# Performance work log

Hardware: AMD Instinct MI355X
Metric: run time of the kernel (lower is better)

The kernel has to match this reference:

```python
import jax, jax.numpy as jnp
import numpy as np

T, B, OBS, H, FC = 128, 512, 1024, 512, 512
LN_EPS = 1e-6  # flax LayerNorm default


def setup_inputs() -> dict:
    key = jax.random.key(0)
    ks = jax.random.split(key, 8)
    sc = lambda k, shape, s: jax.random.normal(k, shape, jnp.float32) * s
    return dict(
        hidden=jnp.zeros((B, H), jnp.float32),  # GRUCell.initialize_carry -> zeros
        world_state=jax.random.normal(ks[0], (T, B, OBS), jnp.float32),
        dones=jax.random.bernoulli(ks[1], 0.05, (T, B)),
        Wd=sc(ks[2], (OBS, H), 1.0 / np.sqrt(OBS)),
        bd=jnp.zeros((H,), jnp.float32),
        ln_scale=jnp.ones((H,), jnp.float32),
        ln_bias=jnp.zeros((H,), jnp.float32),
        Wi=sc(ks[3], (H, 3 * H), 1.0 / np.sqrt(H)),  # input-side GRU weights [r|z|n]
        bi=jnp.zeros((3 * H,), jnp.float32),
        Wh=sc(ks[4], (H, 3 * H), 1.0 / np.sqrt(H)),  # hidden-side GRU weights [r|z|n]
        bhn=jnp.zeros((H,), jnp.float32),            # flax GRU: only hn dense has bias
        Wc1=sc(ks[5], (H, FC), 1.0 / np.sqrt(H)),
        bc1=jnp.zeros((FC,), jnp.float32),
        Wc2=sc(ks[6], (FC, 1), 1.0 / np.sqrt(FC)),
        bc2=jnp.zeros((1,), jnp.float32),
    )


def reference(hidden, world_state, dones, Wd, bd, ln_scale, ln_bias,
              Wi, bi, Wh, bhn, Wc1, bc1, Wc2, bc2):
    # Embed: Dense -> relu -> LayerNorm, applied to all timesteps at once
    emb = jax.nn.relu(world_state @ Wd + bd)                      # [T,B,H]
    mu = emb.mean(-1, keepdims=True)
    var = ((emb - mu) ** 2).mean(-1, keepdims=True)
    emb = (emb - mu) * jax.lax.rsqrt(var + LN_EPS) * ln_scale + ln_bias

    # Precompute input-side GRU projections for all steps (hoisted out of scan)
    xproj = emb @ Wi + bi                                         # [T,B,3H]

    def step(h, inputs):
        xp, done = inputs
        h = jnp.where(done[:, None], 0.0, h)                      # reset carry on done
        xr, xz, xn = jnp.split(xp, 3, axis=-1)
        hr, hz, hn = jnp.split(h @ Wh, 3, axis=-1)                # [B,H] each
        r = jax.nn.sigmoid(xr + hr)
        z = jax.nn.sigmoid(xz + hz)
        n = jnp.tanh(xn + r * (hn + bhn))
        h_new = (1.0 - z) * n + z * h
        return h_new, h_new

    h_last, ys = jax.lax.scan(step, hidden, (xproj, dones))       # ys: [T,B,H]

    critic = jax.nn.relu(ys @ Wc1 + bc1)                          # [T,B,FC]
    value = jnp.squeeze(critic @ Wc2 + bc2, axis=-1)              # [T,B]
    return h_last, value
```

## Files before the change

kernel.cpp:

```cpp
#include <hip/hip_runtime.h>
#include <stdint.h>

#define T_STEPS 128
#define BATCH   512
#define OBSD    1024
#define HD      512
#define FCD     512
#define MROWS   (T_STEPS * BATCH)

typedef unsigned short ushort_t;
typedef __attribute__((ext_vector_type(8))) short bf16x8;
typedef __attribute__((ext_vector_type(4))) float f32x4;

__device__ inline ushort_t f2bf(float f) {
    union { float f; uint32_t u; } v; v.f = f;
    uint32_t r = v.u + 0x7FFFu + ((v.u >> 16) & 1u);
    return (ushort_t)(r >> 16);
}
__device__ inline float bf2f(ushort_t h) {
    union { uint32_t u; float f; } v; v.u = ((uint32_t)h) << 16;
    return v.f;
}
__device__ inline float fsigmoid(float x) {
    x = fminf(fmaxf(x, -30.f), 30.f);
    return 1.f / (1.f + __expf(-x));
}
__device__ inline float ftanh(float x) {
    float e = __expf(fminf(fmaxf(2.f * x, -30.f), 30.f));
    return (e - 1.f) / (e + 1.f);
}

__global__ void transpose_to_bf16(const float* __restrict__ in,
                                  ushort_t* __restrict__ out, int R, int C) {
    __shared__ float tile[32][33];
    int tx = threadIdx.x, ty = threadIdx.y;
    int c0 = blockIdx.x * 32, r0 = blockIdx.y * 32;
    for (int yy = 0; yy < 4; ++yy)
        tile[ty + 8 * yy][tx] = in[(size_t)(r0 + ty + 8 * yy) * C + c0 + tx];
    __syncthreads();
    for (int yy = 0; yy < 4; ++yy)
        out[(size_t)(c0 + ty + 8 * yy) * R + r0 + tx] = f2bf(tile[tx][ty + 8 * yy]);
}

__global__ void init_misc(float* __restrict__ v, const float* __restrict__ bc2,
                          unsigned* __restrict__ bar) {
    int i = blockIdx.x * blockDim.x + threadIdx.x;
    if (i < MROWS) v[i] = bc2[0];
    if (i < 2048) bar[i] = 0u;
}

template <int K, int EPI, bool AF32>
__global__ __launch_bounds__(256) void gemm64(
    const void* __restrict__ Aptr, const ushort_t* __restrict__ BT,
    const float* __restrict__ bias, ushort_t* __restrict__ Cout, int ldc,
    const float* __restrict__ wc2, float* __restrict__ value) {
    __shared__ __align__(16) ushort_t Als[64][40];
    __shared__ __align__(16) ushort_t Bls[64][40];
    int tid = threadIdx.x;
    int wave = tid >> 6, lane = tid & 63, quad = lane >> 4, l16 = lane & 15;
    int bm = blockIdx.x * 64, bn = blockIdx.y * 64;
    int lrow = tid >> 2, lk = (tid & 3) * 8;

    f32x4 acc[4];
    for (int c = 0; c < 4; ++c) acc[c] = (f32x4){0.f, 0.f, 0.f, 0.f};

    for (int k0 = 0; k0 < K; k0 += 32) {
        if constexpr (AF32) {
            const float* A = (const float*)Aptr;
            const float4* pa =
                (const float4*)&A[(size_t)(bm + lrow) * K + k0 + lk];
            float4 a0 = pa[0], a1 = pa[1];
            ushort_t* d = &Als[lrow][lk];
            d[0] = f2bf(a0.x); d[1] = f2bf(a0.y); d[2] = f2bf(a0.z); d[3] = f2bf(a0.w);
            d[4] = f2bf(a1.x); d[5] = f2bf(a1.y); d[6] = f2bf(a1.z); d[7] = f2bf(a1.w);
        } else {
            const ushort_t* A = (const ushort_t*)Aptr;
            *(bf16x8*)&Als[lrow][lk] =
                *(const bf16x8*)&A[(size_t)(bm + lrow) * K + k0 + lk];
        }
        *(bf16x8*)&Bls[lrow][lk] =
            *(const bf16x8*)&BT[(size_t)(bn + lrow) * K + k0 + lk];
        __syncthreads();
        bf16x8 a = *(const bf16x8*)&Als[16 * wave + l16][quad * 8];
        for (int c = 0; c < 4; ++c) {
            bf16x8 b = *(const bf16x8*)&Bls[16 * c + l16][quad * 8];
            acc[c] = __builtin_amdgcn_mfma_f32_16x16x32_bf16(a, b, acc[c], 0, 0, 0);
        }
        __syncthreads();
    }

    int row_l = 16 * wave + 4 * quad;
    if constexpr (EPI == 0 || EPI == 1) {
        for (int c = 0; c < 4; ++c) {
            int col = bn + 16 * c + l16;
            float bv = bias[col];
            for (int i = 0; i < 4; ++i) {
                float v = acc[c][i] + bv;
                if constexpr (EPI == 0) v = fmaxf(v, 0.f);
                Cout[(size_t)(bm + row_l + i) * ldc + col] = f2bf(v);
            }
        }
    } else {
        float s[4] = {0.f, 0.f, 0.f, 0.f};
        for (int c = 0; c < 4; ++c) {
            int col = bn + 16 * c + l16;
            float bv = bias[col], w2 = wc2[col];
            for (int i = 0; i < 4; ++i)
                s[i] += fmaxf(acc[c][i] + bv, 0.f) * w2;
        }
        for (int i = 0; i < 4; ++i) {
            float v = s[i];
            v += __shfl_xor(v, 1);
            v += __shfl_xor(v, 2);
            v += __shfl_xor(v, 4);
            v += __shfl_xor(v, 8);
            if (l16 == 0) atomicAdd(&value[bm + row_l + i], v);
        }
    }
}

__global__ __launch_bounds__(256) void ln_kernel(ushort_t* __restrict__ emb,
                                                 const float* __restrict__ scale,
                                                 const float* __restrict__ biasv) {
    int wave = threadIdx.x >> 6, lane = threadIdx.x & 63;
    size_t row = (size_t)blockIdx.x * 4 + wave;
    ushort_t* p = &emb[row * HD + lane * 8];
    bf16x8 xv = *(const bf16x8*)p;
    float x[8];
    float sum = 0.f, sq = 0.f;
    for (int j = 0; j < 8; ++j) {
        x[j] = bf2f((ushort_t)xv[j]);
        sum += x[j];
        sq += x[j] * x[j];
    }
    for (int off = 32; off > 0; off >>= 1) {
        sum += __shfl_xor(sum, off);
        sq += __shfl_xor(sq, off);
    }
    float mean = sum * (1.f / 512.f);
    float var = fmaxf(sq * (1.f / 512.f) - mean * mean, 0.f);
    float inv = rsqrtf(var + 1e-6f);
    bf16x8 ov;
    for (int j = 0; j < 8; ++j) {
        int col = lane * 8 + j;
        ov[j] = (short)f2bf((x[j] - mean) * inv * scale[col] + biasv[col]);
    }
    *(bf16x8*)p = ov;
}

__global__ __launch_bounds__(256, 1) void scan_coop(
    const float* __restrict__ hidden, const int* __restrict__ dones,
    const ushort_t* __restrict__ WhT, const float* __restrict__ bhn,
    const ushort_t* __restrict__ xproj, ushort_t* __restrict__ ys,
    float* __restrict__ hlast, ushort_t* hb0, ushort_t* hb1,
    unsigned* bar) {
    __shared__ __align__(16) ushort_t Wls[48][520];
    int tid = threadIdx.x;
    int wave = tid >> 6, lane = tid & 63, quad = lane >> 4, l16 = lane & 15;
    int bid = blockIdx.x;
    int bg = bid & 7, cg = bid >> 3;
    int row0 = bg * 64 + wave * 16;
    int col0 = cg * 16;

    for (int idx = tid; idx < 48 * 64; idx += 256) {
        int c = idx >> 6, ck = (idx & 63) * 8;
        int g = c >> 4, lc = c & 15;
        *(bf16x8*)&Wls[c][ck] =
            *(const bf16x8*)&WhT[(size_t)(g * 512 + col0 + lc) * 512 + ck];
    }

    float mast[4];
    int rbase = row0 + quad * 4;
#pragma unroll
    for (int i = 0; i < 4; ++i) {
        float h0 = hidden[(size_t)(rbase + i) * HD + col0 + l16];
        mast[i] = dones[rbase + i] ? 0.f : h0;
    }
    float bhnv = bhn[col0 + l16];

    unsigned* cnt = &bar[bg * 256];
    unsigned* mycnt = &cnt[(cg & 7) * 32];

#pragma unroll
    for (int i = 0; i < 4; ++i) {
        unsigned u = f2bf(mast[i]);
        unsigned p1 = __shfl_xor((int)u, 1);
        unsigned u32 = u | (p1 << 16);
        unsigned hi = __shfl_xor((int)u32, 2);
        if ((l16 & 3) == 0) {
            unsigned long long q =
                (unsigned long long)u32 | ((unsigned long long)hi << 32);
            __hip_atomic_store(
                (unsigned long long*)&hb0[(size_t)(rbase + i) * HD + col0 + l16],
                q, __ATOMIC_RELAXED, __HIP_MEMORY_SCOPE_AGENT);
        }
    }
    float xr[4], xz[4], xn[4];
    int dn_nxt[4];
#pragma unroll
    for (int i = 0; i < 4; ++i) {
        size_t m = (size_t)(rbase + i);
        const ushort_t* xp = &xproj[m * 1536 + col0 + l16];
        xr[i] = bf2f(xp[0]);
        xz[i] = bf2f(xp[512]);
        xn[i] = bf2f(xp[1024]);
        dn_nxt[i] = dones[BATCH + rbase + i];
    }
    __builtin_amdgcn_s_waitcnt(0);
    __syncthreads();
    if (tid == 0)
        __hip_atomic_fetch_add(mycnt, 1u, __ATOMIC_RELAXED,
                               __HIP_MEMORY_SCOPE_AGENT);

    for (int t = 0; t < T_STEPS; ++t) {
        if (tid == 0) {
            unsigned target = 32u * (unsigned)(t + 1);
            for (;;) {
                unsigned s = 0;
#pragma unroll
                for (int c = 0; c < 8; ++c)
                    s += __hip_atomic_load(&cnt[c * 32], __ATOMIC_RELAXED,
                                           __HIP_MEMORY_SCOPE_AGENT);
                if (s >= target) break;
                __builtin_amdgcn_s_sleep(1);
            }
        }
        __syncthreads();
        asm volatile("" ::: "memory");
        ushort_t* rbuf = (t & 1) ? hb1 : hb0;
        ushort_t* wnext = (t & 1) ? hb0 : hb1;

        bf16x8 afr[16];
        {
            const ushort_t* ap =
                &rbuf[(size_t)(row0 + l16) * HD + quad * 8];
            asm volatile(
                "global_load_dwordx4 %0, %16, off sc0 sc1\n\t"
                "global_load_dwordx4 %1, %16, off offset:64 sc0 sc1\n\t"
                "global_load_dwordx4 %2, %16, off offset:128 sc0 sc1\n\t"
                "global_load_dwordx4 %3, %16, off offset:192 sc0 sc1\n\t"
                "global_load_dwordx4 %4, %16, off offset:256 sc0 sc1\n\t"
                "global_load_dwordx4 %5, %16, off offset:320 sc0 sc1\n\t"
                "global_load_dwordx4 %6, %16, off offset:384 sc0 sc1\n\t"
                "global_load_dwordx4 %7, %16, off offset:448 sc0 sc1\n\t"
                "global_load_dwordx4 %8, %16, off offset:512 sc0 sc1\n\t"
                "global_load_dwordx4 %9, %16, off offset:576 sc0 sc1\n\t"
                "global_load_dwordx4 %10, %16, off offset:640 sc0 sc1\n\t"
                "global_load_dwordx4 %11, %16, off offset:704 sc0 sc1\n\t"
                "global_load_dwordx4 %12, %16, off offset:768 sc0 sc1\n\t"
                "global_load_dwordx4 %13, %16, off offset:832 sc0 sc1\n\t"
                "global_load_dwordx4 %14, %16, off offset:896 sc0 sc1\n\t"
                "global_load_dwordx4 %15, %16, off offset:960 sc0 sc1\n\t"
                "s_waitcnt vmcnt(0)"
                : "=&v"(afr[0]), "=&v"(afr[1]), "=&v"(afr[2]), "=&v"(afr[3]),
                  "=&v"(afr[4]), "=&v"(afr[5]), "=&v"(afr[6]), "=&v"(afr[7]),
                  "=&v"(afr[8]), "=&v"(afr[9]), "=&v"(afr[10]), "=&v"(afr[11]),
                  "=&v"(afr[12]), "=&v"(afr[13]), "=&v"(afr[14]), "=&v"(afr[15])
                : "v"(ap)
                : "memory");
        }
        f32x4 aR = (f32x4){0.f, 0.f, 0.f, 0.f};
        f32x4 aZ = (f32x4){0.f, 0.f, 0.f, 0.f};
        f32x4 aN = (f32x4){0.f, 0.f, 0.f, 0.f};
#pragma unroll
        for (int kt = 0; kt < 16; ++kt) {
            bf16x8 bR = *(const bf16x8*)&Wls[l16][kt * 32 + quad * 8];
            bf16x8 bZ = *(const bf16x8*)&Wls[16 + l16][kt * 32 + quad * 8];
            bf16x8 bN = *(const bf16x8*)&Wls[32 + l16][kt * 32 + quad * 8];
            aR = __builtin_amdgcn_mfma_f32_16x16x32_bf16(afr[kt], bR, aR, 0, 0, 0);
            aZ = __builtin_amdgcn_mfma_f32_16x16x32_bf16(afr[kt], bZ, aZ, 0, 0, 0);
            aN = __builtin_amdgcn_mfma_f32_16x16x32_bf16(afr[kt], bN, aN, 0, 0, 0);
        }

        unsigned long long qpk[4];
        float hnew[4];
#pragma unroll
        for (int i = 0; i < 4; ++i) {
            float r = fsigmoid(xr[i] + aR[i]);
            float z = fsigmoid(xz[i] + aZ[i]);
            float n = ftanh(xn[i] + r * (aN[i] + bhnv));
            hnew[i] = (1.f - z) * n + z * mast[i];
            unsigned u = f2bf(hnew[i]);
            unsigned p1 = __shfl_xor((int)u, 1);
            unsigned u32 = u | (p1 << 16);
            unsigned hi = __shfl_xor((int)u32, 2);
            qpk[i] = (unsigned long long)u32 | ((unsigned long long)hi << 32);
            mast[i] = (t < T_STEPS - 1 && dn_nxt[i]) ? 0.f : hnew[i];
        }
        if (t < T_STEPS - 1 && (l16 & 3) == 0) {
#pragma unroll
            for (int i = 0; i < 4; ++i) {
                unsigned long long qp = dn_nxt[i] ? 0ull : qpk[i];
                __hip_atomic_store(
                    (unsigned long long*)&wnext[(size_t)(rbase + i) * HD +
                                                col0 + l16],
                    qp, __ATOMIC_RELAXED, __HIP_MEMORY_SCOPE_AGENT);
            }
        }
        asm volatile("" ::: "memory");
        __builtin_amdgcn_s_waitcnt(0);
        if ((l16 & 3) == 0) {
#pragma unroll
            for (int i = 0; i < 4; ++i) {
                size_t m = (size_t)t * BATCH + rbase + i;
                *(unsigned long long*)&ys[m * HD + col0 + l16] = qpk[i];
            }
        }
        if (t < T_STEPS - 1) {
            int tn = t + 1;
            int td = (t + 2 < T_STEPS) ? t + 2 : T_STEPS - 1;
#pragma unroll
            for (int i = 0; i < 4; ++i) {
                size_t m = (size_t)tn * BATCH + rbase + i;
                const ushort_t* xp = &xproj[m * 1536 + col0 + l16];
                xr[i] = bf2f(xp[0]);
                xz[i] = bf2f(xp[512]);
                xn[i] = bf2f(xp[1024]);
                dn_nxt[i] = dones[td * BATCH + rbase + i];
            }
        }
        asm volatile("" ::: "memory");
        __syncthreads();
        if (tid == 0 && t < T_STEPS - 1)
            __hip_atomic_fetch_add(mycnt, 1u, __ATOMIC_RELAXED,
                                   __HIP_MEMORY_SCOPE_AGENT);
    }
#pragma unroll
    for (int i = 0; i < 4; ++i)
        hlast[(size_t)(rbase + i) * HD + col0 + l16] = mast[i];
}

extern "C" void kernel_launch(void* const* d_in, const int* in_sizes, int n_in,
                              void* d_out, int out_size, void* d_ws,
                              size_t ws_size, hipStream_t stream) {
    const float* hidden      = (const float*)d_in[0];
    const float* world_state = (const float*)d_in[1];
    const int*   dones       = (const int*)d_in[2];
    const float* Wd  = (const float*)d_in[3];
    const float* bd  = (const float*)d_in[4];
    const float* lns = (const float*)d_in[5];
    const float* lnb = (const float*)d_in[6];
    const float* Wi  = (const float*)d_in[7];
    const float* bi  = (const float*)d_in[8];
    const float* Wh  = (const float*)d_in[9];
    const float* bhn = (const float*)d_in[10];
    const float* Wc1 = (const float*)d_in[11];
    const float* bc1 = (const float*)d_in[12];
    const float* Wc2 = (const float*)d_in[13];
    const float* bc2 = (const float*)d_in[14];

    float* out_h = (float*)d_out;
    float* out_v = out_h + BATCH * HD;

    char* ws = (char*)d_ws;
    ushort_t* WdT   = (ushort_t*)(ws + 0);
    ushort_t* WiT   = (ushort_t*)(ws + 1048576);
    ushort_t* WhT   = (ushort_t*)(ws + 2621440);
    ushort_t* Wc1T  = (ushort_t*)(ws + 4194304);
    unsigned* bar   = (unsigned*)(ws + 4718592);
    ushort_t* hb0   = (ushort_t*)(ws + 4726784);
    ushort_t* hb1   = (ushort_t*)(ws + 5251072);
    ushort_t* xproj = (ushort_t*)(ws + 8388608);
    ushort_t* emb   = (ushort_t*)(ws + 209715200);
    ushort_t* ysb   = emb;

    dim3 tb(32, 8);
    transpose_to_bf16<<<dim3(16, 32), tb, 0, stream>>>(Wd, WdT, OBSD, HD);
    transpose_to_bf16<<<dim3(48, 16), tb, 0, stream>>>(Wi, WiT, HD, 1536);
    transpose_to_bf16<<<dim3(48, 16), tb, 0, stream>>>(Wh, WhT, HD, 1536);
    transpose_to_bf16<<<dim3(16, 16), tb, 0, stream>>>(Wc1, Wc1T, HD, FCD);
    init_misc<<<256, 256, 0, stream>>>(out_v, bc2, bar);

    gemm64<OBSD, 0, true><<<dim3(MROWS / 64, HD / 64), 256, 0, stream>>>(
        world_state, WdT, bd, emb, HD, nullptr, nullptr);
    ln_kernel<<<MROWS / 4, 256, 0, stream>>>(emb, lns, lnb);
    gemm64<HD, 1, false><<<dim3(MROWS / 64, 1536 / 64), 256, 0, stream>>>(
        emb, WiT, bi, xproj, 1536, nullptr, nullptr);
    scan_coop<<<dim3(256), dim3(256), 0, stream>>>(
        hidden, dones, WhT, bhn, xproj, ysb, out_h, hb0, hb1, bar);
    gemm64<HD, 2, false><<<dim3(MROWS / 64, FCD / 64), 256, 0, stream>>>(
        ysb, Wc1T, bc1, nullptr, 0, Wc2, out_v);
}
```

Baseline: 1.719 ms.

## Enlarge GEMM tiles to 128x128 with direct global-to-LDS loads

Replaces the 64x64 GEMM tile, where each wave computed a 16x64 strip, with a 128x128 tile in which each wave computes a 64x64 sub-tile using 4x4 MFMA accumulators. Operands now go from global memory straight into LDS via global_load_lds, and the fp32 to bf16 conversion uses the packed v_cvt_pk_bf16 instruction. The grid is reordered so the N dimension varies fastest. This raises arithmetic intensity and cuts LDS and global traffic per flop, at the cost of more registers and an unpadded LDS layout that may cause bank conflicts. The tile is still single-buffered with no prefetch.

```diff
diff --git a/kernel.cpp b/kernel.cpp
--- a/kernel.cpp
+++ b/kernel.cpp
@@ -11,6 +11,7 @@
 typedef unsigned short ushort_t;
 typedef __attribute__((ext_vector_type(8))) short bf16x8;
 typedef __attribute__((ext_vector_type(4))) float f32x4;
+typedef __attribute__((ext_vector_type(2))) uint32_t u32x2;
 
 __device__ inline ushort_t f2bf(float f) {
     union { float f; uint32_t u; } v; v.f = f;
@@ -28,6 +29,16 @@
 __device__ inline float ftanh(float x) {
     float e = __expf(fminf(fmaxf(2.f * x, -30.f), 30.f));
     return (e - 1.f) / (e + 1.f);
+}
+__device__ inline uint32_t cvt_pk_bf16(float lo, float hi) {
+    uint32_t r;
+    asm("v_cvt_pk_bf16_f32 %0, %1, %2" : "=v"(r) : "v"(lo), "v"(hi));
+    return r;
+}
+__device__ inline void gload16(const void* g, void* l) {
+    __builtin_amdgcn_global_load_lds(
+        (const __attribute__((address_space(1))) uint32_t*)g,
+        (__attribute__((address_space(3))) uint32_t*)l, 16, 0, 0);
 }
 
 __global__ void transpose_to_bf16(const float* __restrict__ in,
@@ -50,72 +61,119 @@
 }
 
 template <int K, int EPI, bool AF32>
-__global__ __launch_bounds__(256) void gemm64(
+__global__ __launch_bounds__(256, 2) void gemm128(
     const void* __restrict__ Aptr, const ushort_t* __restrict__ BT,
     const float* __restrict__ bias, ushort_t* __restrict__ Cout, int ldc,
     const float* __restrict__ wc2, float* __restrict__ value) {
-    __shared__ __align__(16) ushort_t Als[64][40];
-    __shared__ __align__(16) ushort_t Bls[64][40];
+    __shared__ __align__(16) ushort_t Als[128][32];
+    __shared__ __align__(16) ushort_t Bls[128][32];
     int tid = threadIdx.x;
     int wave = tid >> 6, lane = tid & 63, quad = lane >> 4, l16 = lane & 15;
-    int bm = blockIdx.x * 64, bn = blockIdx.y * 64;
-    int lrow = tid >> 2, lk = (tid & 3) * 8;
-
-    f32x4 acc[4];
-    for (int c = 0; c < 4; ++c) acc[c] = (f32x4){0.f, 0.f, 0.f, 0.f};
-
+    int wr = wave >> 1, wc = wave & 1;
+    int bm = blockIdx.y * 128, bn = blockIdx.x * 128;
+
+    f32x4 acc[4][4];
+#pragma unroll
+    for (int m = 0; m < 4; ++m)
+#pragma unroll
+        for (int n = 0; n < 4; ++n) acc[m][n] = (f32x4){0.f, 0.f, 0.f, 0.f};
+
+    int srow = tid >> 2;
+    int sk = (tid & 3) * 8;
+    const ushort_t* Bt0 = &BT[(size_t)(bn + srow) * K + sk];
+    const ushort_t* Bt1 = &BT[(size_t)(bn + 64 + srow) * K + sk];
+    char* AlsDst = (char*)&Als[0][0] + tid * 16;
+    char* BlsDst = (char*)&Bls[0][0] + tid * 16;
+    const ushort_t* At0 = nullptr;
+    const ushort_t* At1 = nullptr;
+    if constexpr (!AF32) {
+        const ushort_t* A = (const ushort_t*)Aptr;
+        At0 = &A[(size_t)(bm + srow) * K + sk];
+        At1 = &A[(size_t)(bm + 64 + srow) * K + sk];
+    }
+
+#pragma unroll 1
     for (int k0 = 0; k0 < K; k0 += 32) {
         if constexpr (AF32) {
             const float* A = (const float*)Aptr;
-            const float4* pa =
-                (const float4*)&A[(size_t)(bm + lrow) * K + k0 + lk];
-            float4 a0 = pa[0], a1 = pa[1];
-            ushort_t* d = &Als[lrow][lk];
-            d[0] = f2bf(a0.x); d[1] = f2bf(a0.y); d[2] = f2bf(a0.z); d[3] = f2bf(a0.w);
-            d[4] = f2bf(a1.x); d[5] = f2bf(a1.y); d[6] = f2bf(a1.z); d[7] = f2bf(a1.w);
+#pragma unroll
+            for (int j = 0; j < 4; ++j) {
+                int f = tid + 256 * j;
+                int r = f >> 3, c4 = f & 7;
+                float4 av =
+                    *(const float4*)&A[(size_t)(bm + r) * K + k0 + c4 * 4];
+                u32x2 w;
+                w[0] = cvt_pk_bf16(av.x, av.y);
+                w[1] = cvt_pk_bf16(av.z, av.w);
+                *(u32x2*)&Als[r][c4 * 4] = w;
+            }
         } else {
-            const ushort_t* A = (const ushort_t*)Aptr;
-            *(bf16x8*)&Als[lrow][lk] =
-                *(const bf16x8*)&A[(size_t)(bm + lrow) * K + k0 + lk];
-        }
-        *(bf16x8*)&Bls[lrow][lk] =
-            *(const bf16x8*)&BT[(size_t)(bn + lrow) * K + k0 + lk];
+            gload16(At0 + k0, AlsDst);
+            gload16(At1 + k0, AlsDst + 4096);
+        }
+        gload16(Bt0 + k0, BlsDst);
+        gload16(Bt1 + k0, BlsDst + 4096);
         __syncthreads();
-        bf16x8 a = *(const bf16x8*)&Als[16 * wave + l16][quad * 8];
-        for (int c = 0; c < 4; ++c) {
-            bf16x8 b = *(const bf16x8*)&Bls[16 * c + l16][quad * 8];
-            acc[c] = __builtin_amdgcn_mfma_f32_16x16x32_bf16(a, b, acc[c], 0, 0, 0);
-        }
+
+        bf16x8 af[4], bfr[4];
+#pragma unroll
+        for (int m = 0; m < 4; ++m)
+            af[m] = *(const bf16x8*)&Als[wr * 64 + m * 16 + l16][quad * 8];
+#pragma unroll
+        for (int n = 0; n < 4; ++n)
+            bfr[n] = *(const bf16x8*)&Bls[wc * 64 + n * 16 + l16][quad * 8];
+#pragma unroll
+        for (int m = 0; m < 4; ++m)
+#pragma unroll
+            for (int n = 0; n < 4; ++n)
+                acc[m][n] = __builtin_amdgcn_mfma_f32_16x16x32_bf16(
+                    af[m], bfr[n], acc[m][n], 0, 0, 0);
         __syncthreads();
     }
 
-    int row_l = 16 * wave + 4 * quad;
+    int rbase = bm + wr * 64 + quad * 4;
     if constexpr (EPI == 0 || EPI == 1) {
-        for (int c = 0; c < 4; ++c) {
-            int col = bn + 16 * c + l16;
+#pragma unroll
+        for (int n = 0; n < 4; ++n) {
+            int col = bn + wc * 64 + n * 16 + l16;
             float bv = bias[col];
+#pragma unroll
+            for (int m = 0; m < 4; ++m) {
+#pragma unroll
+                for (int i = 0; i < 4; ++i) {
+                    float v = acc[m][n][i] + bv;
+                    if constexpr (EPI == 0) v = fmaxf(v, 0.f);
+                    Cout[(size_t)(rbase + m * 16 + i) * ldc + col] = f2bf(v);
+                }
+            }
+        }
+    } else {
+        float s[4][4];
+#pragma unroll
+        for (int m = 0; m < 4; ++m)
+#pragma unroll
+            for (int i = 0; i < 4; ++i) s[m][i] = 0.f;
+#pragma unroll
+        for (int n = 0; n < 4; ++n) {
+            int col = bn + wc * 64 + n * 16 + l16;
+            float bv = bias[col], w2 = wc2[col];
+#pragma unroll
+            for (int m = 0; m < 4; ++m)
+#pragma unroll
+                for (int i = 0; i < 4; ++i)
+                    s[m][i] += fmaxf(acc[m][n][i] + bv, 0.f) * w2;
+        }
+#pragma unroll
+        for (int m = 0; m < 4; ++m)
+#pragma unroll
             for (int i = 0; i < 4; ++i) {
-                float v = acc[c][i] + bv;
-                if constexpr (EPI == 0) v = fmaxf(v, 0.f);
-                Cout[(size_t)(bm + row_l + i) * ldc + col] = f2bf(v);
-            }
-        }
-    } else {
-        float s[4] = {0.f, 0.f, 0.f, 0.f};
-        for (int c = 0; c < 4; ++c) {
-            int col = bn + 16 * c + l16;
-            float bv = bias[col], w2 = wc2[col];
-            for (int i = 0; i < 4; ++i)
-                s[i] += fmaxf(acc[c][i] + bv, 0.f) * w2;
-        }
-        for (int i = 0; i < 4; ++i) {
-            float v = s[i];
-            v += __shfl_xor(v, 1);
-            v += __shfl_xor(v, 2);
-            v += __shfl_xor(v, 4);
-            v += __shfl_xor(v, 8);
-            if (l16 == 0) atomicAdd(&value[bm + row_l + i], v);
-        }
+                float v = s[m][i];
+                v += __shfl_xor(v, 1);
+                v += __shfl_xor(v, 2);
+                v += __shfl_xor(v, 4);
+                v += __shfl_xor(v, 8);
+                if (l16 == 0) atomicAdd(&value[rbase + m * 16 + i], v);
+            }
     }
 }
 
@@ -371,13 +429,13 @@
     transpose_to_bf16<<<dim3(16, 16), tb, 0, stream>>>(Wc1, Wc1T, HD, FCD);
     init_misc<<<256, 256, 0, stream>>>(out_v, bc2, bar);
 
-    gemm64<OBSD, 0, true><<<dim3(MROWS / 64, HD / 64), 256, 0, stream>>>(
+    gemm128<OBSD, 0, true><<<dim3(HD / 128, MROWS / 128), 256, 0, stream>>>(
         world_state, WdT, bd, emb, HD, nullptr, nullptr);
     ln_kernel<<<MROWS / 4, 256, 0, stream>>>(emb, lns, lnb);
-    gemm64<HD, 1, false><<<dim3(MROWS / 64, 1536 / 64), 256, 0, stream>>>(
+    gemm128<HD, 1, false><<<dim3(1536 / 128, MROWS / 128), 256, 0, stream>>>(
         emb, WiT, bi, xproj, 1536, nullptr, nullptr);
     scan_coop<<<dim3(256), dim3(256), 0, stream>>>(
         hidden, dones, WhT, bhn, xproj, ysb, out_h, hb0, hb1, bar);
-    gemm64<HD, 2, false><<<dim3(MROWS / 64, FCD / 64), 256, 0, stream>>>(
+    gemm128<HD, 2, false><<<dim3(FCD / 128, MROWS / 128), 256, 0, stream>>>(
         ysb, Wc1T, bc1, nullptr, 0, Wc2, out_v);
 }
```

New measurement: 1.428 ms. 16.9% less time.
